# Performance work log

Measured on AMD Instinct MI355X. Metric: run time of the kernel, lower is better.

The kernel has to match this reference:

```python
import jax, jax.numpy as jnp
import numpy as np

N = 50000      # nodes
E = 800000     # edges (before self-loops)
IN_C = 128
HID = 64
HEADS = 4
OUT_C = 64
NEG_SLOPE = 0.2  # PyG GATConv default


def setup_inputs() -> dict:
    key = jax.random.key(0)
    ks = jax.random.split(key, 12)
    def glorot(k, shape, fan):
        return jax.random.normal(k, shape, jnp.float32) * (1.0 / np.sqrt(fan))
    return {
        "x": jax.random.normal(ks[0], (N, IN_C), jnp.float32),
        "edge_index": jax.random.randint(ks[1], (2, E), 0, N, dtype=jnp.int32),
        # layer 1: in -> heads*hid, concat=True
        "W1": glorot(ks[2], (IN_C, HEADS * HID), IN_C),
        "att1_src": glorot(ks[3], (HEADS, HID), HID),
        "att1_dst": glorot(ks[4], (HEADS, HID), HID),
        "b1": jnp.zeros((HEADS * HID,), jnp.float32),
        # layer 2: heads*hid -> out, heads=1
        "W2": glorot(ks[5], (HEADS * HID, OUT_C), HEADS * HID),
        "att2_src": glorot(ks[6], (1, OUT_C), OUT_C),
        "att2_dst": glorot(ks[7], (1, OUT_C), OUT_C),
        "b2": jnp.zeros((OUT_C,), jnp.float32),
    }


def gat_conv(x, src, dst, W, a_src, a_dst, b, heads):
    """One PyG-style GATConv (self-loops already included in src/dst)."""
    n = x.shape[0]
    c = W.shape[1] // heads
    h = (x @ W).reshape(n, heads, c)                    # [N,H,C]
    alpha_s = jnp.sum(h * a_src, axis=-1)               # [N,H]
    alpha_d = jnp.sum(h * a_dst, axis=-1)               # [N,H]
    e = jax.nn.leaky_relu(alpha_s[src] + alpha_d[dst], NEG_SLOPE)  # [E',H]
    # segment softmax over incoming edges of each destination node
    m = jax.ops.segment_max(e, dst, num_segments=n)
    m = jnp.where(jnp.isfinite(m), m, 0.0)
    ex = jnp.exp(e - m[dst])
    denom = jax.ops.segment_sum(ex, dst, num_segments=n)
    alpha = ex / (denom[dst] + 1e-16)                   # [E',H]
    msg = h[src] * alpha[..., None]                     # [E',H,C]
    out = jax.ops.segment_sum(msg, dst, num_segments=n) # [N,H,C]
    return out.reshape(n, heads * c) + b


def reference(x, edge_index, W1, att1_src, att1_dst, b1, W2, att2_src, att2_dst, b2):
    n = x.shape[0]
    loop = jnp.arange(n, dtype=edge_index.dtype)
    src = jnp.concatenate([edge_index[0], loop])
    dst = jnp.concatenate([edge_index[1], loop])
    # dropout is identity in eval mode
    h = gat_conv(x, src, dst, W1, att1_src, att1_dst, b1, HEADS)
    h = jax.nn.elu(h)
    return gat_conv(h, src, dst, W2, att2_src, att2_dst, b2, 1)
```

## Files before the change

### kernel.cpp

```cpp
#include <hip/hip_runtime.h>
#include <hip/hip_bf16.h>
#include <hip/hip_fp16.h>

#define NNODES 50000
#define NEDGES 800000
#define EPLUS  (NEDGES + NNODES)
#define INC    128
#define HID    64
#define NHEADS 4
#define OUTC   64
#define NEG_SLOPE 0.2f
#define STRIDE 48
#define NSLOTS (NNODES * STRIDE)

typedef __attribute__((ext_vector_type(8))) short short8;
typedef __attribute__((ext_vector_type(4))) float floatx4;

__global__ void k_uvec(const float* __restrict__ W1, const float* __restrict__ a1s,
                       const float* __restrict__ a1d, float* __restrict__ us,
                       float* __restrict__ ud) {
    int i = threadIdx.x + blockIdx.x * blockDim.x;
    if (i >= NHEADS * INC) return;
    int h = i >> 7, k = i & 127;
    const float* wp = W1 + (size_t)k * (NHEADS * HID) + h * HID;
    const float* sp = a1s + h * HID;
    const float* dp = a1d + h * HID;
    float s = 0.f, d = 0.f;
#pragma unroll 8
    for (int c = 0; c < HID; c++) { float w = wp[c]; s += w * sp[c]; d += w * dp[c]; }
    us[i] = s; ud[i] = d;
}

__global__ void k_prep_x(const float* __restrict__ x, const float* __restrict__ us,
                         const float* __restrict__ ud, __hip_bfloat16* __restrict__ xb,
                         float* __restrict__ as1, float* __restrict__ ad1) {
    int w = threadIdx.x >> 6;
    int lane = threadIdx.x & 63;
    int n = blockIdx.x * 4 + w;
    if (n >= NNODES) return;
    float2 xv = *(const float2*)(x + (size_t)n * INC + lane * 2);
    __hip_bfloat16 o[2];
    o[0] = __float2bfloat16(xv.x);
    o[1] = __float2bfloat16(xv.y);
    *(unsigned*)(xb + (size_t)n * INC + lane * 2) = *(unsigned*)o;
    float ps[4], pd[4];
#pragma unroll
    for (int h = 0; h < 4; h++) {
        float2 sv = *(const float2*)(us + h * INC + lane * 2);
        float2 dv = *(const float2*)(ud + h * INC + lane * 2);
        ps[h] = xv.x * sv.x + xv.y * sv.y;
        pd[h] = xv.x * dv.x + xv.y * dv.y;
    }
#pragma unroll
    for (int off = 1; off < 64; off <<= 1) {
#pragma unroll
        for (int h = 0; h < 4; h++) {
            ps[h] += __shfl_xor(ps[h], off, 64);
            pd[h] += __shfl_xor(pd[h], off, 64);
        }
    }
    if (lane == 0) {
        float4 vs = {ps[0], ps[1], ps[2], ps[3]};
        float4 vd = {pd[0], pd[1], pd[2], pd[3]};
        *(float4*)&as1[n * 4] = vs;
        *(float4*)&ad1[n * 4] = vd;
    }
}


__global__ void k_scat_w1(const int* __restrict__ ei, int* __restrict__ cursor,
                          const float* __restrict__ as, const float* __restrict__ ad,
                          int4* __restrict__ rec) {
    int e = blockIdx.x * blockDim.x + threadIdx.x;
    if (e >= EPLUS) return;
    int src, dst;
    if (e < NEDGES) { src = ei[e]; dst = ei[NEDGES + e]; }
    else            { src = dst = e - NEDGES; }
    int slot = atomicAdd(&cursor[dst], 1);
    if (slot >= STRIDE) return;
    int pos = dst * STRIDE + slot;
    float4 sv = *(const float4*)&as[src * 4];
    float4 dv = *(const float4*)&ad[dst * 4];
    float t, w0, w1, w2, w3;
    t = sv.x + dv.x; t = (t > 0.f) ? t : NEG_SLOPE * t; w0 = __expf(t);
    t = sv.y + dv.y; t = (t > 0.f) ? t : NEG_SLOPE * t; w1 = __expf(t);
    t = sv.z + dv.z; t = (t > 0.f) ? t : NEG_SLOPE * t; w2 = __expf(t);
    t = sv.w + dv.w; t = (t > 0.f) ? t : NEG_SLOPE * t; w3 = __expf(t);
    __half2 p01 = __floats2half2_rn(w0, w1);
    __half2 p23 = __floats2half2_rn(w2, w3);
    int4 rc;
    rc.x = src;
    rc.y = *(int*)&p01;
    rc.z = *(int*)&p23;
    rc.w = 0;
    rec[pos] = rc;
}


__global__ void k_agg1n(const __hip_bfloat16* __restrict__ xb, const int* __restrict__ cnt,
                        const int4* __restrict__ rec, __hip_bfloat16* __restrict__ aggb) {
    int w = threadIdx.x >> 6;
    int lane = threadIdx.x & 63;
    int n = blockIdx.x * 4 + w;
    if (n >= NNODES) return;
    int deg = cnt[n]; if (deg > STRIDE) deg = STRIDE;
    int beg = n * STRIDE, end = beg + deg;
    const unsigned* xp = (const unsigned*)xb + lane;

    float accL[4] = {0.f, 0.f, 0.f, 0.f};
    float accH[4] = {0.f, 0.f, 0.f, 0.f};
    float den[4]  = {0.f, 0.f, 0.f, 0.f};

    int j = beg;
    for (; j + 3 < end; j += 4) {
        int4 r0 = rec[j], r1 = rec[j + 1], r2 = rec[j + 2], r3 = rec[j + 3];
        unsigned u0 = xp[(size_t)r0.x * 64];
        unsigned u1 = xp[(size_t)r1.x * 64];
        unsigned u2 = xp[(size_t)r2.x * 64];
        unsigned u3 = xp[(size_t)r3.x * 64];
        int4 rr[4] = {r0, r1, r2, r3};
        unsigned uu[4] = {u0, u1, u2, u3};
#pragma unroll
        for (int q = 0; q < 4; q++) {
            __half2 p01 = *(__half2*)&rr[q].y;
            __half2 p23 = *(__half2*)&rr[q].z;
            float wt[4] = {__low2float(p01), __high2float(p01),
                           __low2float(p23), __high2float(p23)};
            float lo = __uint_as_float(uu[q] << 16);
            float hi = __uint_as_float(uu[q] & 0xffff0000u);
#pragma unroll
            for (int h = 0; h < 4; h++) {
                accL[h] += wt[h] * lo;
                accH[h] += wt[h] * hi;
                den[h]  += wt[h];
            }
        }
    }
    for (; j < end; j++) {
        int4 r0 = rec[j];
        unsigned u0 = xp[(size_t)r0.x * 64];
        __half2 p01 = *(__half2*)&r0.y;
        __half2 p23 = *(__half2*)&r0.z;
        float wt[4] = {__low2float(p01), __high2float(p01),
                       __low2float(p23), __high2float(p23)};
        float lo = __uint_as_float(u0 << 16);
        float hi = __uint_as_float(u0 & 0xffff0000u);
#pragma unroll
        for (int h = 0; h < 4; h++) {
            accL[h] += wt[h] * lo;
            accH[h] += wt[h] * hi;
            den[h]  += wt[h];
        }
    }
#pragma unroll
    for (int h = 0; h < 4; h++) {
        float inv = 1.f / (den[h] + 1e-16f);
        __hip_bfloat16 o[2];
        o[0] = __float2bfloat16(accL[h] * inv);
        o[1] = __float2bfloat16(accH[h] * inv);
        *(unsigned*)(aggb + ((size_t)n * NHEADS + h) * INC + lane * 2) = *(unsigned*)o;
    }
}


__global__ void k_swz1(const float* __restrict__ W1, __hip_bfloat16* __restrict__ Bsw) {
    int i = blockIdx.x * blockDim.x + threadIdx.x;
    if (i >= 4 * 4 * 4 * 64 * 8) return;
    int j = i & 7, l = (i >> 3) & 63, t = (i >> 9) & 3, s = (i >> 11) & 3, h = i >> 13;
    int k = s * 32 + (l >> 4) * 8 + j;
    int col = h * 64 + t * 16 + (l & 15);
    Bsw[i] = __float2bfloat16(W1[(size_t)k * 256 + col]);
}

__global__ void k_swz2(const float* __restrict__ W2, __hip_bfloat16* __restrict__ Bsw) {
    int i = blockIdx.x * blockDim.x + threadIdx.x;
    if (i >= 8 * 4 * 64 * 8) return;
    int j = i & 7, l = (i >> 3) & 63, t = (i >> 9) & 3, s = i >> 11;
    int k = s * 32 + (l >> 4) * 8 + j;
    int col = t * 16 + (l & 15);
    Bsw[i] = __float2bfloat16(W2[(size_t)k * 64 + col]);
}


__global__ void k_mm1(const __hip_bfloat16* __restrict__ A,
                      const __hip_bfloat16* __restrict__ Bsw,
                      const float* __restrict__ b1,
                      __hip_bfloat16* __restrict__ out1b) {
    int row0 = blockIdx.x * 64;
    int h = blockIdx.y;
    int w = threadIdx.x >> 6;
    int l = threadIdx.x & 63;
    int lg = l >> 4, lm = l & 15;
    int ra = row0 + w * 16 + lm;
    if (ra >= NNODES) ra = NNODES - 1;

    floatx4 acc[4];
#pragma unroll
    for (int t = 0; t < 4; t++) acc[t] = (floatx4){0.f, 0.f, 0.f, 0.f};

    const __hip_bfloat16* ap = A + ((size_t)ra * NHEADS + h) * INC + lg * 8;
#pragma unroll
    for (int s = 0; s < 4; s++) {
        short8 a = *(const short8*)(ap + s * 32);
#pragma unroll
        for (int t = 0; t < 4; t++) {
            short8 b = *(const short8*)(Bsw + (((h * 4 + s) * 4 + t) * 64 + l) * 8);
            acc[t] = __builtin_amdgcn_mfma_f32_16x16x32_bf16(a, b, acc[t], 0, 0, 0);
        }
    }
#pragma unroll
    for (int t = 0; t < 4; t++) {
        int col = h * 64 + t * 16 + lm;
        float bias = b1[col];
#pragma unroll
        for (int r = 0; r < 4; r++) {
            int row = row0 + w * 16 + lg * 4 + r;
            if (row < NNODES) {
                float v = acc[t][r] + bias;
                v = (v > 0.f) ? v : (__expf(v) - 1.f);
                out1b[(size_t)row * 256 + col] = __float2bfloat16(v);
            }
        }
    }
}


__global__ void k_mm2(const __hip_bfloat16* __restrict__ A,
                      const __hip_bfloat16* __restrict__ Bsw,
                      const float* __restrict__ a2s, const float* __restrict__ a2d,
                      __hip_bfloat16* __restrict__ h2b,
                      float* __restrict__ as2, float* __restrict__ ad2) {
    int row0 = blockIdx.x * 64;
    int w = threadIdx.x >> 6;
    int l = threadIdx.x & 63;
    int lg = l >> 4, lm = l & 15;
    int ra = row0 + w * 16 + lm;
    if (ra >= NNODES) ra = NNODES - 1;

    floatx4 acc[4];
#pragma unroll
    for (int t = 0; t < 4; t++) acc[t] = (floatx4){0.f, 0.f, 0.f, 0.f};

    const __hip_bfloat16* ap = A + (size_t)ra * 256 + lg * 8;
#pragma unroll
    for (int s = 0; s < 8; s++) {
        short8 a = *(const short8*)(ap + s * 32);
#pragma unroll
        for (int t = 0; t < 4; t++) {
            short8 b = *(const short8*)(Bsw + ((s * 4 + t) * 64 + l) * 8);
            acc[t] = __builtin_amdgcn_mfma_f32_16x16x32_bf16(a, b, acc[t], 0, 0, 0);
        }
    }
    float ps[4] = {0.f, 0.f, 0.f, 0.f};
    float pd[4] = {0.f, 0.f, 0.f, 0.f};
#pragma unroll
    for (int t = 0; t < 4; t++) {
        int col = t * 16 + lm;
        float vs = a2s[col], vd = a2d[col];
#pragma unroll
        for (int r = 0; r < 4; r++) {
            int row = row0 + w * 16 + lg * 4 + r;
            float v = acc[t][r];
            if (row < NNODES) h2b[(size_t)row * OUTC + col] = __float2bfloat16(v);
            ps[r] += v * vs;
            pd[r] += v * vd;
        }
    }
#pragma unroll
    for (int off = 1; off < 16; off <<= 1) {
#pragma unroll
        for (int r = 0; r < 4; r++) {
            ps[r] += __shfl_xor(ps[r], off, 64);
            pd[r] += __shfl_xor(pd[r], off, 64);
        }
    }
    if (lm == 0) {
#pragma unroll
        for (int r = 0; r < 4; r++) {
            int row = row0 + w * 16 + lg * 4 + r;
            if (row < NNODES) { as2[row] = ps[r]; ad2[row] = pd[r]; }
        }
    }
}


__global__ void k_agg2n(const __hip_bfloat16* __restrict__ h2b, const int* __restrict__ cnt,
                        const int4* __restrict__ rec, const float* __restrict__ as2,
                        const float* __restrict__ ad2, const float* __restrict__ b2,
                        float* __restrict__ out) {
    int w = threadIdx.x >> 6;
    int lane = threadIdx.x & 63;
    int n = blockIdx.x * 4 + w;
    if (n >= NNODES) return;
    int deg = cnt[n]; if (deg > STRIDE) deg = STRIDE;
    int beg = n * STRIDE, end = beg + deg;
    float adv = ad2[n];
    const __hip_bfloat16* hp = h2b + lane;

    float acc = 0.f, den = 0.f;
    int j = beg;
    for (; j + 3 < end; j += 4) {
        int s0 = rec[j].x, s1 = rec[j + 1].x, s2 = rec[j + 2].x, s3 = rec[j + 3].x;
        float t0 = as2[s0] + adv, t1 = as2[s1] + adv;
        float t2 = as2[s2] + adv, t3 = as2[s3] + adv;
        float g0 = __bfloat162float(hp[(size_t)s0 * OUTC]);
        float g1 = __bfloat162float(hp[(size_t)s1 * OUTC]);
        float g2 = __bfloat162float(hp[(size_t)s2 * OUTC]);
        float g3 = __bfloat162float(hp[(size_t)s3 * OUTC]);
        t0 = (t0 > 0.f) ? t0 : NEG_SLOPE * t0; float w0 = __expf(t0);
        t1 = (t1 > 0.f) ? t1 : NEG_SLOPE * t1; float w1 = __expf(t1);
        t2 = (t2 > 0.f) ? t2 : NEG_SLOPE * t2; float w2 = __expf(t2);
        t3 = (t3 > 0.f) ? t3 : NEG_SLOPE * t3; float w3 = __expf(t3);
        acc += w0 * g0 + w1 * g1 + w2 * g2 + w3 * g3;
        den += (w0 + w1) + (w2 + w3);
    }
    for (; j < end; j++) {
        int s0 = rec[j].x;
        float t0 = as2[s0] + adv;
        t0 = (t0 > 0.f) ? t0 : NEG_SLOPE * t0;
        float w0 = __expf(t0);
        acc += w0 * __bfloat162float(hp[(size_t)s0 * OUTC]);
        den += w0;
    }
    out[(size_t)n * OUTC + lane] = acc / (den + 1e-16f) + b2[lane];
}


extern "C" void kernel_launch(void* const* d_in, const int* in_sizes, int n_in,
                              void* d_out, int out_size, void* d_ws, size_t ws_size,
                              hipStream_t stream) {
    const float* x   = (const float*)d_in[0];
    const int*   ei  = (const int*)d_in[1];
    const float* W1  = (const float*)d_in[2];
    const float* a1s = (const float*)d_in[3];
    const float* a1d = (const float*)d_in[4];
    const float* b1  = (const float*)d_in[5];
    const float* W2  = (const float*)d_in[6];
    const float* a2s = (const float*)d_in[7];
    const float* a2d = (const float*)d_in[8];
    const float* b2  = (const float*)d_in[9];
    float* out = (float*)d_out;

    char* p = (char*)d_ws;
    auto carve = [&](size_t bytes) -> void* {
        void* r = (void*)p;
        p += (bytes + 255) & ~(size_t)255;
        return r;
    };
    __hip_bfloat16* xb    = (__hip_bfloat16*)carve((size_t)NNODES * INC * 2);
    __hip_bfloat16* aggb  = (__hip_bfloat16*)carve((size_t)NNODES * NHEADS * INC * 2);
    __hip_bfloat16* out1b = (__hip_bfloat16*)carve((size_t)NNODES * 256 * 2);
    __hip_bfloat16* h2b   = (__hip_bfloat16*)carve((size_t)NNODES * OUTC * 2);
    __hip_bfloat16* Bsw1  = (__hip_bfloat16*)carve((size_t)4 * 4 * 4 * 64 * 8 * 2);
    __hip_bfloat16* Bsw2  = (__hip_bfloat16*)carve((size_t)8 * 4 * 64 * 8 * 2);
    float* us      = (float*)carve((size_t)NHEADS * INC * 4);
    float* ud      = (float*)carve((size_t)NHEADS * INC * 4);
    float* as1     = (float*)carve((size_t)NNODES * NHEADS * 4);
    float* ad1     = (float*)carve((size_t)NNODES * NHEADS * 4);
    float* as2     = (float*)carve((size_t)NNODES * 4);
    float* ad2     = (float*)carve((size_t)NNODES * 4);
    int*   cursor  = (int*)carve((size_t)NNODES * 4);
    int4*  rec     = (int4*)carve((size_t)NSLOTS * 16);

    hipMemsetAsync(cursor, 0, (size_t)NNODES * 4, stream);
    k_uvec<<<2, 256, 0, stream>>>(W1, a1s, a1d, us, ud);
    k_prep_x<<<(NNODES + 3) / 4, 256, 0, stream>>>(x, us, ud, xb, as1, ad1);
    k_swz1<<<(4 * 4 * 4 * 64 * 8 + 255) / 256, 256, 0, stream>>>(W1, Bsw1);
    k_swz2<<<(8 * 4 * 64 * 8 + 255) / 256, 256, 0, stream>>>(W2, Bsw2);

    k_scat_w1<<<(EPLUS + 255) / 256, 256, 0, stream>>>(ei, cursor, as1, ad1, rec);

    k_agg1n<<<(NNODES + 3) / 4, 256, 0, stream>>>(xb, cursor, rec, aggb);
    dim3 g1((NNODES + 63) / 64, NHEADS);
    k_mm1<<<g1, 256, 0, stream>>>(aggb, Bsw1, b1, out1b);

    k_mm2<<<(NNODES + 63) / 64, 256, 0, stream>>>(out1b, Bsw2, a2s, a2d, h2b, as2, ad2);
    k_agg2n<<<(NNODES + 3) / 4, 256, 0, stream>>>(h2b, cursor, rec, as2, ad2, b2, out);
}
```

Measured before the change: 283.2 us.

## Fold cursor reset into prep, merge swizzle kernels, two edges per scatter thread

The memset of the per-node cursor array is dropped and replaced by a zeroing store inside k_prep_x. The two weight-swizzle kernels are merged into one launch. The edge-scatter kernel now handles two edges per thread so more atomics and gathers are in flight per thread. The aggregation kernel switches to packed float2 accumulators so the compiler can emit packed FMA. Together these cut launch count and aim for better latency hiding, at the cost of more register pressure and longer per-thread work in the scatter.

```diff
diff --git a/kernel.cpp b/kernel.cpp
--- a/kernel.cpp
+++ b/kernel.cpp
@@ -5,6 +5,7 @@
 #define NNODES 50000
 #define NEDGES 800000
 #define EPLUS  (NEDGES + NNODES)
+#define EHALF  (EPLUS / 2)
 #define INC    128
 #define HID    64
 #define NHEADS 4
@@ -15,6 +16,7 @@
 
 typedef __attribute__((ext_vector_type(8))) short short8;
 typedef __attribute__((ext_vector_type(4))) float floatx4;
+typedef __attribute__((ext_vector_type(2))) float floatx2;
 
 __global__ void k_uvec(const float* __restrict__ W1, const float* __restrict__ a1s,
                        const float* __restrict__ a1d, float* __restrict__ us,
@@ -33,7 +35,8 @@
 
 __global__ void k_prep_x(const float* __restrict__ x, const float* __restrict__ us,
                          const float* __restrict__ ud, __hip_bfloat16* __restrict__ xb,
-                         float* __restrict__ as1, float* __restrict__ ad1) {
+                         float* __restrict__ as1, float* __restrict__ ad1,
+                         int* __restrict__ cursor) {
     int w = threadIdx.x >> 6;
     int lane = threadIdx.x & 63;
     int n = blockIdx.x * 4 + w;
@@ -64,6 +67,7 @@
         float4 vd = {pd[0], pd[1], pd[2], pd[3]};
         *(float4*)&as1[n * 4] = vs;
         *(float4*)&ad1[n * 4] = vd;
+        cursor[n] = 0;
     }
 }
 
@@ -72,28 +76,43 @@
                           const float* __restrict__ as, const float* __restrict__ ad,
                           int4* __restrict__ rec) {
     int e = blockIdx.x * blockDim.x + threadIdx.x;
-    if (e >= EPLUS) return;
-    int src, dst;
-    if (e < NEDGES) { src = ei[e]; dst = ei[NEDGES + e]; }
-    else            { src = dst = e - NEDGES; }
-    int slot = atomicAdd(&cursor[dst], 1);
-    if (slot >= STRIDE) return;
-    int pos = dst * STRIDE + slot;
-    float4 sv = *(const float4*)&as[src * 4];
-    float4 dv = *(const float4*)&ad[dst * 4];
+    if (e >= EHALF) return;
+    int eB = e + EHALF;
+    int srcA, dstA;
+    if (e < NEDGES) { srcA = ei[e]; dstA = ei[NEDGES + e]; }
+    else            { srcA = dstA = e - NEDGES; }
+    int srcB, dstB;
+    if (eB < NEDGES) { srcB = ei[eB]; dstB = ei[NEDGES + eB]; }
+    else             { srcB = dstB = eB - NEDGES; }
+    int slotA = atomicAdd(&cursor[dstA], 1);
+    int slotB = atomicAdd(&cursor[dstB], 1);
+    float4 svA = *(const float4*)&as[srcA * 4];
+    float4 dvA = *(const float4*)&ad[dstA * 4];
+    float4 svB = *(const float4*)&as[srcB * 4];
+    float4 dvB = *(const float4*)&ad[dstB * 4];
     float t, w0, w1, w2, w3;
-    t = sv.x + dv.x; t = (t > 0.f) ? t : NEG_SLOPE * t; w0 = __expf(t);
-    t = sv.y + dv.y; t = (t > 0.f) ? t : NEG_SLOPE * t; w1 = __expf(t);
-    t = sv.z + dv.z; t = (t > 0.f) ? t : NEG_SLOPE * t; w2 = __expf(t);
-    t = sv.w + dv.w; t = (t > 0.f) ? t : NEG_SLOPE * t; w3 = __expf(t);
-    __half2 p01 = __floats2half2_rn(w0, w1);
-    __half2 p23 = __floats2half2_rn(w2, w3);
-    int4 rc;
-    rc.x = src;
-    rc.y = *(int*)&p01;
-    rc.z = *(int*)&p23;
-    rc.w = 0;
-    rec[pos] = rc;
+    if (slotA < STRIDE) {
+        t = svA.x + dvA.x; t = (t > 0.f) ? t : NEG_SLOPE * t; w0 = __expf(t);
+        t = svA.y + dvA.y; t = (t > 0.f) ? t : NEG_SLOPE * t; w1 = __expf(t);
+        t = svA.z + dvA.z; t = (t > 0.f) ? t : NEG_SLOPE * t; w2 = __expf(t);
+        t = svA.w + dvA.w; t = (t > 0.f) ? t : NEG_SLOPE * t; w3 = __expf(t);
+        __half2 p01 = __floats2half2_rn(w0, w1);
+        __half2 p23 = __floats2half2_rn(w2, w3);
+        int4 rc;
+        rc.x = srcA; rc.y = *(int*)&p01; rc.z = *(int*)&p23; rc.w = 0;
+        rec[dstA * STRIDE + slotA] = rc;
+    }
+    if (slotB < STRIDE) {
+        t = svB.x + dvB.x; t = (t > 0.f) ? t : NEG_SLOPE * t; w0 = __expf(t);
+        t = svB.y + dvB.y; t = (t > 0.f) ? t : NEG_SLOPE * t; w1 = __expf(t);
+        t = svB.z + dvB.z; t = (t > 0.f) ? t : NEG_SLOPE * t; w2 = __expf(t);
+        t = svB.w + dvB.w; t = (t > 0.f) ? t : NEG_SLOPE * t; w3 = __expf(t);
+        __half2 p01 = __floats2half2_rn(w0, w1);
+        __half2 p23 = __floats2half2_rn(w2, w3);
+        int4 rc;
+        rc.x = srcB; rc.y = *(int*)&p01; rc.z = *(int*)&p23; rc.w = 0;
+        rec[dstB * STRIDE + slotB] = rc;
+    }
 }
 
 
@@ -107,9 +126,10 @@
     int beg = n * STRIDE, end = beg + deg;
     const unsigned* xp = (const unsigned*)xb + lane;
 
-    float accL[4] = {0.f, 0.f, 0.f, 0.f};
-    float accH[4] = {0.f, 0.f, 0.f, 0.f};
-    float den[4]  = {0.f, 0.f, 0.f, 0.f};
+    floatx2 acc[4];
+#pragma unroll
+    for (int h = 0; h < 4; h++) acc[h] = (floatx2){0.f, 0.f};
+    float den[4] = {0.f, 0.f, 0.f, 0.f};
 
     int j = beg;
     for (; j + 3 < end; j += 4) {
@@ -126,13 +146,12 @@
             __half2 p23 = *(__half2*)&rr[q].z;
             float wt[4] = {__low2float(p01), __high2float(p01),
                            __low2float(p23), __high2float(p23)};
-            float lo = __uint_as_float(uu[q] << 16);
-            float hi = __uint_as_float(uu[q] & 0xffff0000u);
+            floatx2 xv = {__uint_as_float(uu[q] << 16),
+                          __uint_as_float(uu[q] & 0xffff0000u)};
 #pragma unroll
             for (int h = 0; h < 4; h++) {
-                accL[h] += wt[h] * lo;
-                accH[h] += wt[h] * hi;
-                den[h]  += wt[h];
+                acc[h] += (floatx2){wt[h], wt[h]} * xv;
+                den[h] += wt[h];
             }
         }
     }
@@ -143,42 +162,41 @@
         __half2 p23 = *(__half2*)&r0.z;
         float wt[4] = {__low2float(p01), __high2float(p01),
                        __low2float(p23), __high2float(p23)};
-        float lo = __uint_as_float(u0 << 16);
-        float hi = __uint_as_float(u0 & 0xffff0000u);
+        floatx2 xv = {__uint_as_float(u0 << 16),
+                      __uint_as_float(u0 & 0xffff0000u)};
 #pragma unroll
         for (int h = 0; h < 4; h++) {
-            accL[h] += wt[h] * lo;
-            accH[h] += wt[h] * hi;
-            den[h]  += wt[h];
+            acc[h] += (floatx2){wt[h], wt[h]} * xv;
+            den[h] += wt[h];
         }
     }
 #pragma unroll
     for (int h = 0; h < 4; h++) {
         float inv = 1.f / (den[h] + 1e-16f);
         __hip_bfloat16 o[2];
-        o[0] = __float2bfloat16(accL[h] * inv);
-        o[1] = __float2bfloat16(accH[h] * inv);
+        o[0] = __float2bfloat16(acc[h].x * inv);
+        o[1] = __float2bfloat16(acc[h].y * inv);
         *(unsigned*)(aggb + ((size_t)n * NHEADS + h) * INC + lane * 2) = *(unsigned*)o;
     }
 }
 
 
-__global__ void k_swz1(const float* __restrict__ W1, __hip_bfloat16* __restrict__ Bsw) {
+__global__ void k_swz12(const float* __restrict__ W1, const float* __restrict__ W2,
+                        __hip_bfloat16* __restrict__ Bsw1, __hip_bfloat16* __restrict__ Bsw2) {
     int i = blockIdx.x * blockDim.x + threadIdx.x;
-    if (i >= 4 * 4 * 4 * 64 * 8) return;
-    int j = i & 7, l = (i >> 3) & 63, t = (i >> 9) & 3, s = (i >> 11) & 3, h = i >> 13;
-    int k = s * 32 + (l >> 4) * 8 + j;
-    int col = h * 64 + t * 16 + (l & 15);
-    Bsw[i] = __float2bfloat16(W1[(size_t)k * 256 + col]);
-}
-
-__global__ void k_swz2(const float* __restrict__ W2, __hip_bfloat16* __restrict__ Bsw) {
-    int i = blockIdx.x * blockDim.x + threadIdx.x;
-    if (i >= 8 * 4 * 64 * 8) return;
-    int j = i & 7, l = (i >> 3) & 63, t = (i >> 9) & 3, s = i >> 11;
-    int k = s * 32 + (l >> 4) * 8 + j;
-    int col = t * 16 + (l & 15);
-    Bsw[i] = __float2bfloat16(W2[(size_t)k * 64 + col]);
+    if (blockIdx.y == 0) {
+        if (i >= 4 * 4 * 4 * 64 * 8) return;
+        int j = i & 7, l = (i >> 3) & 63, t = (i >> 9) & 3, s = (i >> 11) & 3, h = i >> 13;
+        int k = s * 32 + (l >> 4) * 8 + j;
+        int col = h * 64 + t * 16 + (l & 15);
+        Bsw1[i] = __float2bfloat16(W1[(size_t)k * 256 + col]);
+    } else {
+        if (i >= 8 * 4 * 64 * 8) return;
+        int j = i & 7, l = (i >> 3) & 63, t = (i >> 9) & 3, s = i >> 11;
+        int k = s * 32 + (l >> 4) * 8 + j;
+        int col = t * 16 + (l & 15);
+        Bsw2[i] = __float2bfloat16(W2[(size_t)k * 64 + col]);
+    }
 }
 
 
@@ -362,13 +380,12 @@
     int*   cursor  = (int*)carve((size_t)NNODES * 4);
     int4*  rec     = (int4*)carve((size_t)NSLOTS * 16);
 
-    hipMemsetAsync(cursor, 0, (size_t)NNODES * 4, stream);
     k_uvec<<<2, 256, 0, stream>>>(W1, a1s, a1d, us, ud);
-    k_prep_x<<<(NNODES + 3) / 4, 256, 0, stream>>>(x, us, ud, xb, as1, ad1);
-    k_swz1<<<(4 * 4 * 4 * 64 * 8 + 255) / 256, 256, 0, stream>>>(W1, Bsw1);
-    k_swz2<<<(8 * 4 * 64 * 8 + 255) / 256, 256, 0, stream>>>(W2, Bsw2);
-
-    k_scat_w1<<<(EPLUS + 255) / 256, 256, 0, stream>>>(ei, cursor, as1, ad1, rec);
+    k_prep_x<<<(NNODES + 3) / 4, 256, 0, stream>>>(x, us, ud, xb, as1, ad1, cursor);
+    dim3 gsw(128, 2);
+    k_swz12<<<gsw, 256, 0, stream>>>(W1, W2, Bsw1, Bsw2);
+
+    k_scat_w1<<<(EHALF + 255) / 256, 256, 0, stream>>>(ei, cursor, as1, ad1, rec);
 
     k_agg1n<<<(NNODES + 3) / 4, 256, 0, stream>>>(xb, cursor, rec, aggb);
     dim3 g1((NNODES + 63) / 64, NHEADS);
```

Result: faster. 277.3 us, median of 2 (-2.1%).
